# Performance work log

Hardware: AMD Instinct MI355X
Metric: run time of the kernel (lower is better)

The kernel has to match this reference:

```python
import jax, jax.numpy as jnp
import numpy as np

B, S, D, F, E, NS, K = 2, 2048, 512, 2048, 8, 2, 2


def setup_inputs() -> dict:
    key = jax.random.key(0)
    ks = jax.random.split(key, 6)
    scale = 0.02

    def p(k, shape):
        return jax.random.normal(k, shape, jnp.float32) * scale

    return {
        "x": jax.random.normal(ks[0], (B, S, D), jnp.float32),
        "gate_w": p(ks[1], (E, D)),
        "gate_b": jnp.zeros((E,), jnp.float32),
        "sw1": p(ks[2], (NS, F, D)),
        "sb1": jnp.zeros((NS, F), jnp.float32),
        "sw2": p(ks[3], (NS, D, F)),
        "sb2": jnp.zeros((NS, D), jnp.float32),
        "rw1": p(ks[4], (E, F, D)),
        "rb1": jnp.zeros((E, F), jnp.float32),
        "rw2": p(ks[5], (E, D, F)),
        "rb2": jnp.zeros((E, D), jnp.float32),
    }


def reference(x, gate_w, gate_b, sw1, sb1, sw2, sb2, rw1, rb1, rw2, rb2):
    b, s, d = x.shape
    t = x.reshape(-1, d)  # [T, D] flatten batch*seq tokens
    T = t.shape[0]

    # ---- shared experts: sum over NS FFNs (GELU exact, matching nn.GELU) ----
    hs = jax.nn.gelu(jnp.einsum('td,nfd->ntf', t, sw1) + sb1[:, None, :],
                     approximate=False)
    shared = jnp.einsum('ntf,ndf->td', hs, sw2) + sb2.sum(axis=0)

    # ---- router: softmax over experts, top-k probs/indices ----
    logits = t @ gate_w.T + gate_b               # [T, E]
    probs = jax.nn.softmax(logits, axis=-1)
    top_v, top_i = jax.lax.top_k(probs, K)       # [T, K]

    # combine weights: cw[t, e] = sum_k top_v[t, k] * (top_i[t, k] == e)
    cw = jnp.zeros_like(probs).at[jnp.arange(T)[:, None], top_i].add(top_v)  # [T, E]

    # ---- routed experts: run each expert FFN over all tokens, combine by cw ----
    # Mathematically identical to the masked gather/scatter loop in the source:
    # tokens with cw[t,e]==0 contribute nothing.
    hr = jax.nn.gelu(jnp.einsum('td,efd->etf', t, rw1) + rb1[:, None, :],
                     approximate=False)          # [E, T, F]
    oe = jnp.einsum('etf,edf->etd', hr, rw2) + rb2[:, None, :]  # [E, T, D]
    routed = jnp.einsum('etd,te->td', oe, cw)    # weighted combine

    return (shared + routed).reshape(b, s, d)
```

## Files before the change

### kernel.cpp

```cpp
#include <hip/hip_runtime.h>
#include <math.h>

typedef unsigned short u16;
typedef __attribute__((ext_vector_type(8))) __bf16 bf16x8;
typedef __attribute__((ext_vector_type(4))) float floatx4;

#define T_TOK 4096
#define DD    512
#define FF    2048
#define EE    8
#define NSH   2

#define BM 128
#define BN 128
#define BK 32
#define LDK 40
#define LDK2 32
#define BT2 64
#define CAP 4096
#define PADF 0x80000000u
#define NSLOT (2 * T_TOK + EE * BM)

__device__ __forceinline__ float bf2f(u16 v) {
  union { unsigned int u; float f; } c; c.u = ((unsigned int)v) << 16; return c.f;
}
__device__ __forceinline__ u16 f2bf(float f) {
  union { float ff; unsigned int u; } c; c.ff = f;
  unsigned int u = c.u;
  u += 0x7fffu + ((u >> 16) & 1u);
  return (u16)(u >> 16);
}
__device__ __forceinline__ float decode(const void* p, size_t idx, int f) {
  return f ? ((const float*)p)[idx] : bf2f(((const u16*)p)[idx]);
}
__device__ __forceinline__ bf16x8 load8(const void* base, size_t idx, int f) {
  if (f) {
    const float* p = (const float*)base + idx;
    float4 a = *(const float4*)p;
    float4 b = *(const float4*)(p + 4);
    union { bf16x8 v; u16 s[8]; } u;
    u.s[0] = f2bf(a.x); u.s[1] = f2bf(a.y); u.s[2] = f2bf(a.z); u.s[3] = f2bf(a.w);
    u.s[4] = f2bf(b.x); u.s[5] = f2bf(b.y); u.s[6] = f2bf(b.z); u.s[7] = f2bf(b.w);
    return u.v;
  }
  return *(const bf16x8*)((const u16*)base + idx);
}
__device__ __forceinline__ void loadf8(const void* p, size_t idx, int f,
                                       float* o) {
  if (f) {
    const float* q = (const float*)p + idx;
    float4 a = *(const float4*)q;
    float4 b = *(const float4*)(q + 4);
    o[0] = a.x; o[1] = a.y; o[2] = a.z; o[3] = a.w;
    o[4] = b.x; o[5] = b.y; o[6] = b.z; o[7] = b.w;
  } else {
    union { bf16x8 v; u16 s[8]; } u;
    u.v = *(const bf16x8*)((const u16*)p + idx);
#pragma unroll
    for (int j = 0; j < 8; ++j) o[j] = bf2f(u.s[j]);
  }
}

__device__ __forceinline__ float fast_gelu(float v) {
  float x  = v * 0.70710678118654752f;
  float ax = fabsf(x);
  float t  = __builtin_amdgcn_rcpf(fmaf(0.3275911f, ax, 1.0f));
  float p  = fmaf(t, 1.061405429f, -1.453152027f);
  p = fmaf(t, p, 1.421413741f);
  p = fmaf(t, p, -0.284496736f);
  p = fmaf(t, p, 0.254829592f);
  p = p * t;
  float e  = __expf(-ax * ax);
  float er = fmaf(-p, e, 1.0f);
  er = (x < 0.f) ? -er : er;
  return 0.5f * v * (1.0f + er);
}

__device__ __forceinline__ void gll16(const void* g, void* l) {
  __builtin_amdgcn_global_load_lds(
      (const __attribute__((address_space(1))) void*)g,
      (__attribute__((address_space(3))) void*)l, 16, 0, 0);
}
__device__ __forceinline__ void stage4(const u16* gA0, const u16* gA1,
                                       const u16* gB0, const u16* gB1,
                                       u16* Asb, u16* Bsb, int wave, int k0) {
  gll16(gA0 + k0, Asb + wave * 512);
  gll16(gA1 + k0, Asb + 2048 + wave * 512);
  gll16(gB0 + k0, Bsb + wave * 512);
  gll16(gB1 + k0, Bsb + 2048 + wave * 512);
}

__global__ __launch_bounds__(256) void detect_kernel(
    const void* x, const void* gw, const void* sw1, const void* sw2,
    const void* rw1, const void* rw2, int* flags, int* meta) {
  __shared__ int cnt;
  __shared__ int sflags[6];
  const void* ptrs[6] = {x, gw, sw1, sw2, rw1, rw2};
  for (int tnum = 0; tnum < 6; ++tnum) {
    if (threadIdx.x == 0) cnt = 0;
    __syncthreads();
    const u16* p = (const u16*)ptrs[tnum];
    int local = 0;
    for (int i = threadIdx.x; i < 4096; i += 256) {
      unsigned ef = (p[i] >> 7) & 0xFFu;
      if (ef >= 0xE0u) ++local;
    }
    if (local) atomicAdd(&cnt, local);
    __syncthreads();
    if (threadIdx.x == 0) sflags[tnum] = (cnt >= 16) ? 1 : 0;
    __syncthreads();
  }
  if (threadIdx.x == 0) {
#pragma unroll
    for (int i = 0; i < 6; ++i) flags[i] = sflags[i];
    flags[6] = sflags[0];
    flags[7] = 0;
  }
  if (meta && threadIdx.x < 24) meta[threadIdx.x] = 0;
}

__global__ __launch_bounds__(256) void conv_kernel(
    const void* __restrict__ src, u16* __restrict__ dst,
    const int* __restrict__ flags, int idx, size_t n) {
  int f = flags[idx];
  size_t i = ((size_t)blockIdx.x * 256 + threadIdx.x) * 8;
  if (i >= n) return;
  *(bf16x8*)(dst + i) = load8(src, i, f);
}

__global__ __launch_bounds__(256) void router_v(
    const void* __restrict__ x, const void* __restrict__ gw,
    const u16* __restrict__ gb, const int* __restrict__ flags,
    float* __restrict__ cw, int2* __restrict__ tix) {
  int wave = threadIdx.x >> 6, lane = threadIdx.x & 63;
  int t = blockIdx.x * 4 + wave;
  int fx = flags[0], fg = flags[1];
  float xf[8];
  loadf8(x, (size_t)t * DD + lane * 8, fx, xf);
  float acc[EE];
#pragma unroll
  for (int e = 0; e < EE; ++e) {
    float gf[8];
    loadf8(gw, (size_t)e * DD + lane * 8, fg, gf);
    float a = 0.f;
#pragma unroll
    for (int j = 0; j < 8; ++j) a = fmaf(xf[j], gf[j], a);
    acc[e] = a;
  }
#pragma unroll
  for (int e = 0; e < EE; ++e) {
    float v = acc[e];
#pragma unroll
    for (int off = 32; off > 0; off >>= 1) v += __shfl_xor(v, off, 64);
    acc[e] = v;
  }
  if (lane == 0) {
    float m = -1e30f;
#pragma unroll
    for (int e = 0; e < EE; ++e) {
      acc[e] += bf2f(gb[e]);
      m = fmaxf(m, acc[e]);
    }
    float p[EE], s = 0.f;
#pragma unroll
    for (int e = 0; e < EE; ++e) { p[e] = expf(acc[e] - m); s += p[e]; }
    int i1 = 0;
#pragma unroll
    for (int e = 1; e < EE; ++e) if (p[e] > p[i1]) i1 = e;
    int i2 = (i1 == 0) ? 1 : 0;
#pragma unroll
    for (int e = 0; e < EE; ++e)
      if (e != i1 && p[e] > p[i2]) i2 = e;
    float inv = 1.0f / s;
#pragma unroll
    for (int e = 0; e < EE; ++e)
      cw[t * EE + e] = (e == i1 || e == i2) ? p[e] * inv : 0.0f;
    tix[t] = make_int2(i1, i2);
  }
}

__global__ __launch_bounds__(256) void build_lists(
    const int2* __restrict__ tix, int* __restrict__ meta,
    unsigned* __restrict__ list, int4* __restrict__ srec) {
  int t = blockIdx.x * 256 + threadIdx.x;
  if (t >= T_TOK) return;
  int2 ii = tix[t];
  int p0 = atomicAdd(&meta[ii.x], 1);
  list[(size_t)ii.x * CAP + p0] = (unsigned)t;
  int p1 = atomicAdd(&meta[ii.y], 1);
  list[(size_t)ii.y * CAP + p1] = (unsigned)t;
  srec[t] = make_int4(ii.x, p0, ii.y, p1);
}
__global__ __launch_bounds__(256) void pad_lists(int* meta, unsigned* list) {
  if (threadIdx.x == 0) {
    int off = 0;
    for (int e = 0; e < EE; ++e) {
      int c = meta[e];
      int pc = (c + BM - 1) & ~(BM - 1);
      meta[8 + e] = pc;
      meta[16 + e] = off;
      off += pc;
    }
  }
  __syncthreads();
#pragma unroll
  for (int e = 0; e < EE; ++e) {
    int c = meta[e], pc = meta[8 + e];
    int i = c + threadIdx.x;
    if (i < pc) list[(size_t)e * CAP + i] = PADF;
  }
}


__global__ __launch_bounds__(256) void g1_fused(
    const u16* __restrict__ xb, const u16* __restrict__ s1b,
    const u16* __restrict__ sb1, const u16* __restrict__ r1b,
    const u16* __restrict__ rb1, const unsigned* __restrict__ list,
    const int* __restrict__ meta, u16* __restrict__ Hsh,
    u16* __restrict__ Hrt) {
  int z = blockIdx.z;
  int bm = blockIdx.y * BM;
  int tid = threadIdx.x, lane = tid & 63, wave = tid >> 6;
  int wm = (wave >> 1) * 64, wn = (wave & 1) * 64;
  int r = lane & 15, q = lane >> 4;
  int srow = tid >> 2, sc8 = (tid & 3) * 8;
  const int K = DD;

  __shared__ u16 As[2][BM * LDK2];
  __shared__ u16 Bs[2][BN * LDK2];

  const u16 *gA0, *gA1, *gB0;
  int e = 0, ho = 0, bn;
  if (z < 2) {
    bn = (z * 16 + blockIdx.x) * BN;
    gA0 = xb + (size_t)(bm + srow) * K + sc8;
    gA1 = gA0 + (size_t)64 * K;
    gB0 = s1b + (size_t)(bn + srow) * K + sc8;
  } else {
    e = z - 2;
    if (bm >= meta[8 + e]) return;
    ho = meta[16 + e];
    bn = blockIdx.x * BN;
    unsigned t0 = list[(size_t)e * CAP + bm + srow] & 0x7fffffffu;
    unsigned t1 = list[(size_t)e * CAP + bm + srow + 64] & 0x7fffffffu;
    gA0 = xb + (size_t)t0 * K + sc8;
    gA1 = xb + (size_t)t1 * K + sc8;
    gB0 = r1b + (size_t)e * FF * DD + (size_t)(bn + srow) * K + sc8;
  }
  const u16* gB1 = gB0 + (size_t)64 * K;

  floatx4 acc[4][4];
  floatx4 zero = {0.f, 0.f, 0.f, 0.f};
#pragma unroll
  for (int i = 0; i < 4; ++i)
#pragma unroll
    for (int j = 0; j < 4; ++j) acc[i][j] = zero;

  stage4(gA0, gA1, gB0, gB1, As[0], Bs[0], wave, 0);
  __syncthreads();
  int cur = 0;
  for (int k0 = 0; k0 < K; k0 += BK) {
    if (k0 + BK < K)
      stage4(gA0, gA1, gB0, gB1, As[cur ^ 1], Bs[cur ^ 1], wave, k0 + BK);
    bf16x8 af[4], bfr[4];
#pragma unroll
    for (int mi = 0; mi < 4; ++mi)
      af[mi] = *(const bf16x8*)(As[cur] + (wm + mi * 16 + r) * LDK2 + q * 8);
#pragma unroll
    for (int ni = 0; ni < 4; ++ni)
      bfr[ni] = *(const bf16x8*)(Bs[cur] + (wn + ni * 16 + r) * LDK2 + q * 8);
#pragma unroll
    for (int mi = 0; mi < 4; ++mi)
#pragma unroll
      for (int ni = 0; ni < 4; ++ni)
        acc[mi][ni] = __builtin_amdgcn_mfma_f32_16x16x32_bf16(
            af[mi], bfr[ni], acc[mi][ni], 0, 0, 0);
    __syncthreads();
    cur ^= 1;
  }

  if (z < 2) {
#pragma unroll
    for (int mi = 0; mi < 4; ++mi)
#pragma unroll
      for (int ni = 0; ni < 4; ++ni) {
        int col = bn + wn + ni * 16 + r;
        float bv = bf2f(sb1[col]);
#pragma unroll
        for (int rr = 0; rr < 4; ++rr) {
          int row = bm + wm + mi * 16 + q * 4 + rr;
          float v = acc[mi][ni][rr] + bv;
          Hsh[(size_t)row * (NSH * FF) + col] = f2bf(fast_gelu(v));
        }
      }
  } else {
#pragma unroll
    for (int mi = 0; mi < 4; ++mi)
#pragma unroll
      for (int ni = 0; ni < 4; ++ni) {
        int col = bn + wn + ni * 16 + r;
        float bv = bf2f(rb1[(size_t)e * FF + col]);
#pragma unroll
        for (int rr = 0; rr < 4; ++rr) {
          int slot = bm + wm + mi * 16 + q * 4 + rr;
          float v = acc[mi][ni][rr] + bv;
          Hrt[(size_t)(ho + slot) * FF + col] = f2bf(fast_gelu(v));
        }
      }
  }
}

__global__ __launch_bounds__(256) void g2_fused(
    const u16* __restrict__ Hsh, const u16* __restrict__ s2b,
    const u16* __restrict__ sb2, const u16* __restrict__ Hrt,
    const u16* __restrict__ r2b, const u16* __restrict__ rb2,
    const unsigned* __restrict__ list, const int* __restrict__ meta,
    const float* __restrict__ cw, float* __restrict__ oacc,
    float* __restrict__ Ort) {
  int z = blockIdx.z;
  int bm = blockIdx.y * BM;
  int bn = blockIdx.x * BN;
  int tid = threadIdx.x, lane = tid & 63, wave = tid >> 6;
  int wm = (wave >> 1) * 64, wn = (wave & 1) * 64;
  int r = lane & 15, q = lane >> 4;
  int srow = tid >> 2, sc8 = (tid & 3) * 8;
  const int K = FF;

  __shared__ u16 As[2][BM * LDK2];
  __shared__ u16 Bs[2][BN * LDK2];

  const u16 *gA0, *gA1, *gB0;
  int e = 0, ho = 0;
  if (z < NSH) {
    gA0 = Hsh + (size_t)(bm + srow) * (NSH * FF) + (size_t)z * FF + sc8;
    gA1 = gA0 + (size_t)64 * (NSH * FF);
    gB0 = s2b + (size_t)z * DD * FF + (size_t)(bn + srow) * K + sc8;
  } else {
    e = z - NSH;
    if (bm >= meta[8 + e]) return;
    ho = meta[16 + e];
    gA0 = Hrt + (size_t)(ho + bm + srow) * K + sc8;
    gA1 = gA0 + (size_t)64 * K;
    gB0 = r2b + (size_t)e * DD * FF + (size_t)(bn + srow) * K + sc8;
  }
  const u16* gB1 = gB0 + (size_t)64 * K;

  floatx4 acc[4][4];
  floatx4 zero = {0.f, 0.f, 0.f, 0.f};
#pragma unroll
  for (int i = 0; i < 4; ++i)
#pragma unroll
    for (int j = 0; j < 4; ++j) acc[i][j] = zero;

  stage4(gA0, gA1, gB0, gB1, As[0], Bs[0], wave, 0);
  __syncthreads();
  int cur = 0;
  for (int k0 = 0; k0 < K; k0 += BK) {
    if (k0 + BK < K)
      stage4(gA0, gA1, gB0, gB1, As[cur ^ 1], Bs[cur ^ 1], wave, k0 + BK);
    bf16x8 af[4], bfr[4];
#pragma unroll
    for (int mi = 0; mi < 4; ++mi)
      af[mi] = *(const bf16x8*)(As[cur] + (wm + mi * 16 + r) * LDK2 + q * 8);
#pragma unroll
    for (int ni = 0; ni < 4; ++ni)
      bfr[ni] = *(const bf16x8*)(Bs[cur] + (wn + ni * 16 + r) * LDK2 + q * 8);
#pragma unroll
    for (int mi = 0; mi < 4; ++mi)
#pragma unroll
      for (int ni = 0; ni < 4; ++ni)
        acc[mi][ni] = __builtin_amdgcn_mfma_f32_16x16x32_bf16(
            af[mi], bfr[ni], acc[mi][ni], 0, 0, 0);
    __syncthreads();
    cur ^= 1;
  }

  if (z < NSH) {
    float* op = oacc + (size_t)z * T_TOK * DD;
#pragma unroll
    for (int mi = 0; mi < 4; ++mi)
#pragma unroll
      for (int ni = 0; ni < 4; ++ni) {
        int col = bn + wn + ni * 16 + r;
        float bv = bf2f(sb2[(size_t)z * DD + col]);
#pragma unroll
        for (int rr = 0; rr < 4; ++rr) {
          int row = bm + wm + mi * 16 + q * 4 + rr;
          op[(size_t)row * DD + col] = acc[mi][ni][rr] + bv;
        }
      }
  } else {
#pragma unroll
    for (int mi = 0; mi < 4; ++mi)
#pragma unroll
      for (int rr = 0; rr < 4; ++rr) {
        int slot = bm + wm + mi * 16 + q * 4 + rr;
        unsigned raw = list[(size_t)e * CAP + slot];
        if (raw & PADF) continue;
        float s = cw[raw * EE + e];
#pragma unroll
        for (int ni = 0; ni < 4; ++ni) {
          int col = bn + wn + ni * 16 + r;
          float v = acc[mi][ni][rr] + bf2f(rb2[(size_t)e * DD + col]);
          Ort[(size_t)(ho + slot) * DD + col] = s * v;
        }
      }
  }
}

typedef struct { u16 a, b, c, d; } u16x4;
__global__ __launch_bounds__(256) void combine_out(
    const float* __restrict__ oacc, const float* __restrict__ Ort,
    const int4* __restrict__ srec, const int* __restrict__ meta,
    void* __restrict__ out, const int* __restrict__ flags) {
  int t  = blockIdx.x * 2 + (threadIdx.x >> 7);
  int c4 = (threadIdx.x & 127) * 4;
  int4 sr = srec[t];
  int g0 = meta[16 + sr.x] + sr.y;
  int g1 = meta[16 + sr.z] + sr.w;
  float4 a = *(const float4*)(oacc + (size_t)t * DD + c4);
  float4 b = *(const float4*)(oacc + (size_t)(T_TOK + t) * DD + c4);
  float4 u = *(const float4*)(Ort + (size_t)g0 * DD + c4);
  float4 v = *(const float4*)(Ort + (size_t)g1 * DD + c4);
  float o0 = a.x + b.x + u.x + v.x;
  float o1 = a.y + b.y + u.y + v.y;
  float o2 = a.z + b.z + u.z + v.z;
  float o3 = a.w + b.w + u.w + v.w;
  size_t idx = (size_t)t * DD + c4;
  if (flags[6]) {
    *(float4*)((float*)out + idx) = make_float4(o0, o1, o2, o3);
  } else {
    u16x4 h = {f2bf(o0), f2bf(o1), f2bf(o2), f2bf(o3)};
    *(u16x4*)((u16*)out + idx) = h;
  }
}

__device__ __forceinline__ void gemm_core(const void* A, size_t aoff, int fA,
                                          const void* B, size_t boff, int fB,
                                          int K, u16* As, u16* Bs,
                                          floatx4 acc[4][4]) {
  int tid  = threadIdx.x;
  int lane = tid & 63, wave = tid >> 6;
  int wm = (wave >> 1) * 64, wn = (wave & 1) * 64;
  int r = lane & 15, q = lane >> 4;
  int srow = tid >> 2;
  int sc8  = (tid & 3) * 8;
  size_t abase = aoff + (size_t)srow * K + sc8;
  size_t bbase = boff + (size_t)srow * K + sc8;
  const size_t half = (size_t)64 * K;

  for (int k0 = 0; k0 < K; k0 += BK) {
    bf16x8 av0 = load8(A, abase + k0, fA);
    bf16x8 av1 = load8(A, abase + half + k0, fA);
    bf16x8 bv0 = load8(B, bbase + k0, fB);
    bf16x8 bv1 = load8(B, bbase + half + k0, fB);
    __syncthreads();
    *(bf16x8*)(As + srow * LDK + sc8)        = av0;
    *(bf16x8*)(As + (srow + 64) * LDK + sc8) = av1;
    *(bf16x8*)(Bs + srow * LDK + sc8)        = bv0;
    *(bf16x8*)(Bs + (srow + 64) * LDK + sc8) = bv1;
    __syncthreads();

    bf16x8 af[4], bfr[4];
#pragma unroll
    for (int mi = 0; mi < 4; ++mi)
      af[mi] = *(const bf16x8*)(As + (wm + mi * 16 + r) * LDK + q * 8);
#pragma unroll
    for (int ni = 0; ni < 4; ++ni)
      bfr[ni] = *(const bf16x8*)(Bs + (wn + ni * 16 + r) * LDK + q * 8);
#pragma unroll
    for (int mi = 0; mi < 4; ++mi)
#pragma unroll
      for (int ni = 0; ni < 4; ++ni)
        acc[mi][ni] = __builtin_amdgcn_mfma_f32_16x16x32_bf16(
            af[mi], bfr[ni], acc[mi][ni], 0, 0, 0);
  }
}

__global__ __launch_bounds__(256) void gemm1_gelu(
    const void* __restrict__ A, size_t aoff, const void* __restrict__ B,
    size_t boff, const u16* __restrict__ bias, size_t bioff,
    u16* __restrict__ H, const int* __restrict__ flags, int iA, int iB,
    int N, int K) {
  __shared__ u16 As[BM * LDK];
  __shared__ u16 Bs[BN * LDK];
  int fA = flags[iA], fB = flags[iB];
  floatx4 acc[4][4];
  floatx4 zero = {0.f, 0.f, 0.f, 0.f};
#pragma unroll
  for (int i = 0; i < 4; ++i)
#pragma unroll
    for (int j = 0; j < 4; ++j) acc[i][j] = zero;

  int bm = blockIdx.y * BM, bn = blockIdx.x * BN;
  gemm_core(A, aoff + (size_t)bm * K, fA, B, boff + (size_t)bn * K, fB, K,
            As, Bs, acc);

  int tid = threadIdx.x, wave = tid >> 6, lane = tid & 63;
  int wm = (wave >> 1) * 64, wn = (wave & 1) * 64;
  int r = lane & 15, q = lane >> 4;
#pragma unroll
  for (int mi = 0; mi < 4; ++mi)
#pragma unroll
    for (int ni = 0; ni < 4; ++ni) {
      int col = bn + wn + ni * 16 + r;
      float bv = bf2f(bias[bioff + col]);
#pragma unroll
      for (int rr = 0; rr < 4; ++rr) {
        int row = bm + wm + mi * 16 + q * 4 + rr;
        float v = acc[mi][ni][rr] + bv;
        H[(size_t)row * N + col] = f2bf(fast_gelu(v));
      }
    }
}

__global__ __launch_bounds__(256) void gemm2_acc(
    const u16* __restrict__ A, const void* __restrict__ B, size_t boff,
    const u16* __restrict__ bias, size_t bioff, float* __restrict__ outf,
    void* __restrict__ outb, const float* __restrict__ cw,
    const int* __restrict__ flags, int iB, int expert, int accum,
    int row0, int N, int K) {
  __shared__ u16 As[BT2 * LDK];
  __shared__ u16 Bs[BT2 * LDK];
  int fB = flags[iB], fO = flags[6];
  floatx4 acc[2][2];
  floatx4 zero = {0.f, 0.f, 0.f, 0.f};
#pragma unroll
  for (int i = 0; i < 2; ++i)
#pragma unroll
    for (int j = 0; j < 2; ++j) acc[i][j] = zero;

  int bm = blockIdx.y * BT2, bn = blockIdx.x * BT2;
  int tid  = threadIdx.x;
  int lane = tid & 63, wave = tid >> 6;
  int wm = (wave >> 1) * 32, wn = (wave & 1) * 32;
  int r = lane & 15, q = lane >> 4;
  int srow = tid >> 2;
  int sc8  = (tid & 3) * 8;
  size_t abase = (size_t)(bm + srow) * K + sc8;
  size_t bbase = boff + (size_t)(bn + srow) * K + sc8;

  for (int k0 = 0; k0 < K; k0 += BK) {
    bf16x8 av = *(const bf16x8*)(A + abase + k0);
    bf16x8 bv = load8(B, bbase + k0, fB);
    __syncthreads();
    *(bf16x8*)(As + srow * LDK + sc8) = av;
    *(bf16x8*)(Bs + srow * LDK + sc8) = bv;
    __syncthreads();

    bf16x8 af[2], bfr[2];
#pragma unroll
    for (int mi = 0; mi < 2; ++mi)
      af[mi] = *(const bf16x8*)(As + (wm + mi * 16 + r) * LDK + q * 8);
#pragma unroll
    for (int ni = 0; ni < 2; ++ni)
      bfr[ni] = *(const bf16x8*)(Bs + (wn + ni * 16 + r) * LDK + q * 8);
#pragma unroll
    for (int mi = 0; mi < 2; ++mi)
#pragma unroll
      for (int ni = 0; ni < 2; ++ni)
        acc[mi][ni] = __builtin_amdgcn_mfma_f32_16x16x32_bf16(
            af[mi], bfr[ni], acc[mi][ni], 0, 0, 0);
  }

#pragma unroll
  for (int mi = 0; mi < 2; ++mi)
#pragma unroll
    for (int rr = 0; rr < 4; ++rr) {
      int grow = row0 + bm + wm + mi * 16 + q * 4 + rr;
      float s = cw ? cw[grow * EE + expert] : 1.0f;
#pragma unroll
      for (int ni = 0; ni < 2; ++ni) {
        int col = bn + wn + ni * 16 + r;
        float v = acc[mi][ni][rr] + bf2f(bias[bioff + col]);
        size_t idx = (size_t)grow * N + col;
        if (outf) {
          float prev = accum ? outf[idx] : 0.0f;
          outf[idx] = prev + s * v;
        } else if (fO) {
          float* ob = (float*)outb;
          float prev = accum ? ob[idx] : 0.0f;
          ob[idx] = prev + s * v;
        } else {
          u16* ob = (u16*)outb;
          float prev = accum ? bf2f(ob[idx]) : 0.0f;
          ob[idx] = f2bf(prev + s * v);
        }
      }
    }
}

__global__ __launch_bounds__(256) void convert_out(
    const float* __restrict__ acc, void* __restrict__ out,
    const int* __restrict__ flags, int n) {
  int i = blockIdx.x * blockDim.x + threadIdx.x;
  if (i >= n) return;
  if (flags[6]) ((float*)out)[i] = acc[i];
  else ((u16*)out)[i] = f2bf(acc[i]);
}

extern "C" void kernel_launch(void* const* d_in, const int* in_sizes, int n_in,
                              void* d_out, int out_size, void* d_ws, size_t ws_size,
                              hipStream_t stream) {
  (void)in_sizes; (void)n_in; (void)out_size;
  const void* x   = d_in[0];
  const void* gw  = d_in[1];
  const u16*  gb  = (const u16*)d_in[2];
  const void* sw1 = d_in[3];
  const u16*  sb1 = (const u16*)d_in[4];
  const void* sw2 = d_in[5];
  const u16*  sb2 = (const u16*)d_in[6];
  const void* rw1 = d_in[7];
  const u16*  rb1 = (const u16*)d_in[8];
  const void* rw2 = d_in[9];
  const u16*  rb2 = (const u16*)d_in[10];

  const size_t NX   = (size_t)T_TOK * DD;
  const size_t NW1S = (size_t)NSH * FF * DD;
  const size_t NW1R = (size_t)EE * FF * DD;
  const size_t NW2S = (size_t)NSH * DD * FF;
  const size_t NW2R = (size_t)EE * DD * FF;

  size_t off = 0;
  const size_t flO   = off; off += 256;
  const size_t cwO   = off; off += (size_t)T_TOK * EE * 4;
  const size_t tixO  = off; off += (size_t)T_TOK * 8;
  const size_t metaO = off; off += 256;
  const size_t listO = off; off += (size_t)EE * CAP * 4;
  const size_t srecO = off; off += (size_t)T_TOK * 16;
  const size_t accO  = off; off += (size_t)NSH * T_TOK * DD * 4;
  const size_t hshO  = off; off += (size_t)T_TOK * NSH * FF * 2;
  const size_t hrtO  = off; off += (size_t)NSLOT * FF * 2;
  const size_t ortO  = off; off += (size_t)NSLOT * DD * 4;
  const size_t xbO   = off; off += NX * 2;
  const size_t s1O   = off; off += NW1S * 2;
  const size_t r1O   = off; off += NW1R * 2;
  const size_t s2O   = off; off += NW2S * 2;
  const size_t r2O   = off; off += NW2R * 2;
  const int fast = (off <= ws_size) ? 1 : 0;

  char* ws = (char*)d_ws;
  int*   flags = (int*)(ws + flO);
  float* cw    = (float*)(ws + cwO);
  dim3 blk(256);

  if (fast) {
    int2*     tix  = (int2*)(ws + tixO);
    int*      meta = (int*)(ws + metaO);
    unsigned* list = (unsigned*)(ws + listO);
    int4*     srec = (int4*)(ws + srecO);
    float*    oacc = (float*)(ws + accO);
    u16*      Hsh  = (u16*)(ws + hshO);
    u16*      Hrt  = (u16*)(ws + hrtO);
    float*    Ort  = (float*)(ws + ortO);
    u16*      xb   = (u16*)(ws + xbO);
    u16*      s1b  = (u16*)(ws + s1O);
    u16*      r1b  = (u16*)(ws + r1O);
    u16*      s2b  = (u16*)(ws + s2O);
    u16*      r2b  = (u16*)(ws + r2O);

    detect_kernel<<<1, 256, 0, stream>>>(x, gw, sw1, sw2, rw1, rw2, flags,
                                         meta);
    conv_kernel<<<NX   / 2048, 256, 0, stream>>>(x,   xb,  flags, 0, NX);
    conv_kernel<<<NW1S / 2048, 256, 0, stream>>>(sw1, s1b, flags, 2, NW1S);
    conv_kernel<<<NW1R / 2048, 256, 0, stream>>>(rw1, r1b, flags, 4, NW1R);
    conv_kernel<<<NW2S / 2048, 256, 0, stream>>>(sw2, s2b, flags, 3, NW2S);
    conv_kernel<<<NW2R / 2048, 256, 0, stream>>>(rw2, r2b, flags, 5, NW2R);
    router_v<<<T_TOK / 4, 256, 0, stream>>>(x, gw, gb, flags, cw, tix);
    build_lists<<<T_TOK / 256, 256, 0, stream>>>(tix, meta, list, srec);
    pad_lists<<<1, 256, 0, stream>>>(meta, list);

    dim3 gf1(16, T_TOK / BM, 2 + EE);
    g1_fused<<<gf1, blk, 0, stream>>>(xb, s1b, sb1, r1b, rb1, list, meta,
                                      Hsh, Hrt);
    dim3 gf2(DD / BN, CAP / BM, NSH + EE);
    g2_fused<<<gf2, blk, 0, stream>>>(Hsh, s2b, sb2, Hrt, r2b, rb2, list,
                                      meta, cw, oacc, Ort);
    combine_out<<<T_TOK / 2, 256, 0, stream>>>(oacc, Ort, srec, meta, d_out,
                                               flags);
    return;
  }

  detect_kernel<<<1, 256, 0, stream>>>(x, gw, sw1, sw2, rw1, rw2, flags,
                                       nullptr);
  const size_t flB = 256, cwB = (size_t)T_TOK * EE * 4, tixB = (size_t)T_TOK * 8;
  const size_t accB = (size_t)T_TOK * DD * 4;
  static const int tcs[4] = {4096, 2048, 1024, 512};
  int TC = 0, use_f32 = 1;
  for (int i = 0; i < 4; ++i)
    if (flB + cwB + tixB + accB + (size_t)tcs[i] * FF * 2 <= ws_size) { TC = tcs[i]; break; }
  if (!TC) {
    use_f32 = 0;
    for (int i = 0; i < 4; ++i)
      if (flB + cwB + tixB + (size_t)tcs[i] * FF * 2 <= ws_size) { TC = tcs[i]; break; }
  }
  if (!TC) { TC = 512; use_f32 = 0; }

  int2*  tix     = (int2*)(ws + flB + cwB);
  float* out_acc = use_f32 ? (float*)(ws + flB + cwB + tixB) : nullptr;
  u16*   H       = (u16*)(ws + flB + cwB + tixB + (use_f32 ? accB : 0));

  router_v<<<T_TOK / 4, 256, 0, stream>>>(x, gw, gb, flags, cw, tix);
  dim3 g1(FF / BN, TC / BM);
  dim3 g2(DD / BT2, TC / BT2);
  const int nchunk = T_TOK / TC;
  for (int f = 0; f < NSH + EE; ++f) {
    const void *w1, *w2; const u16 *b1, *b2; const float* cwp;
    int expert, i1, i2v; size_t w1off, w2off, b1off, b2off;
    if (f < NSH) {
      w1 = sw1; w2 = sw2; b1 = sb1; b2 = sb2;
      w1off = (size_t)f * FF * DD; w2off = (size_t)f * DD * FF;
      b1off = (size_t)f * FF; b2off = (size_t)f * DD;
      cwp = nullptr; expert = 0; i1 = 2; i2v = 3;
    } else {
      int e = f - NSH;
      w1 = rw1; w2 = rw2; b1 = rb1; b2 = rb2;
      w1off = (size_t)e * FF * DD; w2off = (size_t)e * DD * FF;
      b1off = (size_t)e * FF; b2off = (size_t)e * DD;
      cwp = cw; expert = e; i1 = 4; i2v = 5;
    }
    int accum = (f > 0) ? 1 : 0;
    for (int c = 0; c < nchunk; ++c) {
      size_t t0 = (size_t)c * TC;
      gemm1_gelu<<<g1, blk, 0, stream>>>(x, t0 * DD, w1, w1off, b1, b1off, H,
                                         flags, 0, i1, FF, DD);
      gemm2_acc<<<g2, blk, 0, stream>>>(H, w2, w2off, b2, b2off, out_acc,
                                        d_out, cwp, flags, i2v, expert, accum,
                                        (int)t0, DD, FF);
    }
  }
  if (use_f32)
    convert_out<<<(T_TOK * DD) / 256, 256, 0, stream>>>(out_acc, d_out, flags,
                                                        T_TOK * DD);
}
```

Before: 381.5 us.

## Skip bf16 conversion when inputs are already bf16 and single-buffer GEMM LDS

The conversion kernels now return early when the detect flag says no conversion is needed. The two GEMM kernels then read the raw input pointers directly instead of the converted workspace copies, which removes a full copy pass over the weights in that case. The GEMM main loop moves into a shared helper that uses one LDS buffer with a barrier before and after each stage, instead of the double-buffered prefetch. That halves shared memory per block, which may raise occupancy, but global loads can no longer overlap the MFMA work. With fp32 inputs the conversions likely still run, so only the loss of overlap would apply.

```diff
diff --git a/kernel.cpp b/kernel.cpp
--- a/kernel.cpp
+++ b/kernel.cpp
@@ -90,6 +90,31 @@
   gll16(gB1 + k0, Bsb + 2048 + wave * 512);
 }
 
+__device__ __forceinline__ void core128(const u16* gA0, const u16* gA1,
+                                        const u16* gB0, const u16* gB1,
+                                        int K, u16* As, u16* Bs,
+                                        floatx4 acc[4][4], int wave,
+                                        int wm, int wn, int r, int q) {
+  for (int k0 = 0; k0 < K; k0 += BK) {
+    __syncthreads();
+    stage4(gA0, gA1, gB0, gB1, As, Bs, wave, k0);
+    __syncthreads();
+    bf16x8 af[4], bfr[4];
+#pragma unroll
+    for (int mi = 0; mi < 4; ++mi)
+      af[mi] = *(const bf16x8*)(As + (wm + mi * 16 + r) * LDK2 + q * 8);
+#pragma unroll
+    for (int ni = 0; ni < 4; ++ni)
+      bfr[ni] = *(const bf16x8*)(Bs + (wn + ni * 16 + r) * LDK2 + q * 8);
+#pragma unroll
+    for (int mi = 0; mi < 4; ++mi)
+#pragma unroll
+      for (int ni = 0; ni < 4; ++ni)
+        acc[mi][ni] = __builtin_amdgcn_mfma_f32_16x16x32_bf16(
+            af[mi], bfr[ni], acc[mi][ni], 0, 0, 0);
+  }
+}
+
 __global__ __launch_bounds__(256) void detect_kernel(
     const void* x, const void* gw, const void* sw1, const void* sw2,
     const void* rw1, const void* rw2, int* flags, int* meta) {
@@ -123,6 +148,7 @@
     const void* __restrict__ src, u16* __restrict__ dst,
     const int* __restrict__ flags, int idx, size_t n) {
   int f = flags[idx];
+  if (!f) return;
   size_t i = ((size_t)blockIdx.x * 256 + threadIdx.x) * 8;
   if (i >= n) return;
   *(bf16x8*)(dst + i) = load8(src, i, f);
@@ -213,11 +239,17 @@
 
 
 __global__ __launch_bounds__(256) void g1_fused(
-    const u16* __restrict__ xb, const u16* __restrict__ s1b,
-    const u16* __restrict__ sb1, const u16* __restrict__ r1b,
+    const void* __restrict__ xr, const u16* __restrict__ xb,
+    const void* __restrict__ s1r, const u16* __restrict__ s1b,
+    const u16* __restrict__ sb1,
+    const void* __restrict__ r1r, const u16* __restrict__ r1b,
     const u16* __restrict__ rb1, const unsigned* __restrict__ list,
-    const int* __restrict__ meta, u16* __restrict__ Hsh,
-    u16* __restrict__ Hrt) {
+    const int* __restrict__ meta, const int* __restrict__ flags,
+    u16* __restrict__ Hsh, u16* __restrict__ Hrt) {
+  const u16* xp  = flags[0] ? xb  : (const u16*)xr;
+  const u16* s1p = flags[2] ? s1b : (const u16*)s1r;
+  const u16* r1p = flags[4] ? r1b : (const u16*)r1r;
+
   int z = blockIdx.z;
   int bm = blockIdx.y * BM;
   int tid = threadIdx.x, lane = tid & 63, wave = tid >> 6;
@@ -226,16 +258,16 @@
   int srow = tid >> 2, sc8 = (tid & 3) * 8;
   const int K = DD;
 
-  __shared__ u16 As[2][BM * LDK2];
-  __shared__ u16 Bs[2][BN * LDK2];
+  __shared__ u16 As[BM * LDK2];
+  __shared__ u16 Bs[BN * LDK2];
 
   const u16 *gA0, *gA1, *gB0;
   int e = 0, ho = 0, bn;
   if (z < 2) {
     bn = (z * 16 + blockIdx.x) * BN;
-    gA0 = xb + (size_t)(bm + srow) * K + sc8;
+    gA0 = xp + (size_t)(bm + srow) * K + sc8;
     gA1 = gA0 + (size_t)64 * K;
-    gB0 = s1b + (size_t)(bn + srow) * K + sc8;
+    gB0 = s1p + (size_t)(bn + srow) * K + sc8;
   } else {
     e = z - 2;
     if (bm >= meta[8 + e]) return;
@@ -243,9 +275,9 @@
     bn = blockIdx.x * BN;
     unsigned t0 = list[(size_t)e * CAP + bm + srow] & 0x7fffffffu;
     unsigned t1 = list[(size_t)e * CAP + bm + srow + 64] & 0x7fffffffu;
-    gA0 = xb + (size_t)t0 * K + sc8;
-    gA1 = xb + (size_t)t1 * K + sc8;
-    gB0 = r1b + (size_t)e * FF * DD + (size_t)(bn + srow) * K + sc8;
+    gA0 = xp + (size_t)t0 * K + sc8;
+    gA1 = xp + (size_t)t1 * K + sc8;
+    gB0 = r1p + (size_t)e * FF * DD + (size_t)(bn + srow) * K + sc8;
   }
   const u16* gB1 = gB0 + (size_t)64 * K;
 
@@ -256,28 +288,7 @@
 #pragma unroll
     for (int j = 0; j < 4; ++j) acc[i][j] = zero;
 
-  stage4(gA0, gA1, gB0, gB1, As[0], Bs[0], wave, 0);
-  __syncthreads();
-  int cur = 0;
-  for (int k0 = 0; k0 < K; k0 += BK) {
-    if (k0 + BK < K)
-      stage4(gA0, gA1, gB0, gB1, As[cur ^ 1], Bs[cur ^ 1], wave, k0 + BK);
-    bf16x8 af[4], bfr[4];
-#pragma unroll
-    for (int mi = 0; mi < 4; ++mi)
-      af[mi] = *(const bf16x8*)(As[cur] + (wm + mi * 16 + r) * LDK2 + q * 8);
-#pragma unroll
-    for (int ni = 0; ni < 4; ++ni)
-      bfr[ni] = *(const bf16x8*)(Bs[cur] + (wn + ni * 16 + r) * LDK2 + q * 8);
-#pragma unroll
-    for (int mi = 0; mi < 4; ++mi)
-#pragma unroll
-      for (int ni = 0; ni < 4; ++ni)
-        acc[mi][ni] = __builtin_amdgcn_mfma_f32_16x16x32_bf16(
-            af[mi], bfr[ni], acc[mi][ni], 0, 0, 0);
-    __syncthreads();
-    cur ^= 1;
-  }
+  core128(gA0, gA1, gB0, gB1, K, As, Bs, acc, wave, wm, wn, r, q);
 
   if (z < 2) {
 #pragma unroll
@@ -311,12 +322,17 @@
 }
 
 __global__ __launch_bounds__(256) void g2_fused(
-    const u16* __restrict__ Hsh, const u16* __restrict__ s2b,
+    const u16* __restrict__ Hsh,
+    const void* __restrict__ s2r, const u16* __restrict__ s2b,
     const u16* __restrict__ sb2, const u16* __restrict__ Hrt,
-    const u16* __restrict__ r2b, const u16* __restrict__ rb2,
+    const void* __restrict__ r2r, const u16* __restrict__ r2b,
+    const u16* __restrict__ rb2,
     const unsigned* __restrict__ list, const int* __restrict__ meta,
-    const float* __restrict__ cw, float* __restrict__ oacc,
-    float* __restrict__ Ort) {
+    const int* __restrict__ flags, const float* __restrict__ cw,
+    float* __restrict__ oacc, float* __restrict__ Ort) {
+  const u16* s2p = flags[3] ? s2b : (const u16*)s2r;
+  const u16* r2p = flags[5] ? r2b : (const u16*)r2r;
+
   int z = blockIdx.z;
   int bm = blockIdx.y * BM;
   int bn = blockIdx.x * BN;
@@ -326,22 +342,22 @@
   int srow = tid >> 2, sc8 = (tid & 3) * 8;
   const int K = FF;
 
-  __shared__ u16 As[2][BM * LDK2];
-  __shared__ u16 Bs[2][BN * LDK2];
+  __shared__ u16 As[BM * LDK2];
+  __shared__ u16 Bs[BN * LDK2];
 
   const u16 *gA0, *gA1, *gB0;
   int e = 0, ho = 0;
   if (z < NSH) {
     gA0 = Hsh + (size_t)(bm + srow) * (NSH * FF) + (size_t)z * FF + sc8;
     gA1 = gA0 + (size_t)64 * (NSH * FF);
-    gB0 = s2b + (size_t)z * DD * FF + (size_t)(bn + srow) * K + sc8;
+    gB0 = s2p + (size_t)z * DD * FF + (size_t)(bn + srow) * K + sc8;
   } else {
     e = z - NSH;
     if (bm >= meta[8 + e]) return;
     ho = meta[16 + e];
     gA0 = Hrt + (size_t)(ho + bm + srow) * K + sc8;
     gA1 = gA0 + (size_t)64 * K;
-    gB0 = r2b + (size_t)e * DD * FF + (size_t)(bn + srow) * K + sc8;
+    gB0 = r2p + (size_t)e * DD * FF + (size_t)(bn + srow) * K + sc8;
   }
   const u16* gB1 = gB0 + (size_t)64 * K;
 
@@ -352,28 +368,7 @@
 #pragma unroll
     for (int j = 0; j < 4; ++j) acc[i][j] = zero;
 
-  stage4(gA0, gA1, gB0, gB1, As[0], Bs[0], wave, 0);
-  __syncthreads();
-  int cur = 0;
-  for (int k0 = 0; k0 < K; k0 += BK) {
-    if (k0 + BK < K)
-      stage4(gA0, gA1, gB0, gB1, As[cur ^ 1], Bs[cur ^ 1], wave, k0 + BK);
-    bf16x8 af[4], bfr[4];
-#pragma unroll
-    for (int mi = 0; mi < 4; ++mi)
-      af[mi] = *(const bf16x8*)(As[cur] + (wm + mi * 16 + r) * LDK2 + q * 8);
-#pragma unroll
-    for (int ni = 0; ni < 4; ++ni)
-      bfr[ni] = *(const bf16x8*)(Bs[cur] + (wn + ni * 16 + r) * LDK2 + q * 8);
-#pragma unroll
-    for (int mi = 0; mi < 4; ++mi)
-#pragma unroll
-      for (int ni = 0; ni < 4; ++ni)
-        acc[mi][ni] = __builtin_amdgcn_mfma_f32_16x16x32_bf16(
-            af[mi], bfr[ni], acc[mi][ni], 0, 0, 0);
-    __syncthreads();
-    cur ^= 1;
-  }
+  core128(gA0, gA1, gB0, gB1, K, As, Bs, acc, wave, wm, wn, r, q);
 
   if (z < NSH) {
     float* op = oacc + (size_t)z * T_TOK * DD;
@@ -671,11 +666,11 @@
     pad_lists<<<1, 256, 0, stream>>>(meta, list);
 
     dim3 gf1(16, T_TOK / BM, 2 + EE);
-    g1_fused<<<gf1, blk, 0, stream>>>(xb, s1b, sb1, r1b, rb1, list, meta,
-                                      Hsh, Hrt);
+    g1_fused<<<gf1, blk, 0, stream>>>(x, xb, sw1, s1b, sb1, rw1, r1b, rb1,
+                                      list, meta, flags, Hsh, Hrt);
     dim3 gf2(DD / BN, CAP / BM, NSH + EE);
-    g2_fused<<<gf2, blk, 0, stream>>>(Hsh, s2b, sb2, Hrt, r2b, rb2, list,
-                                      meta, cw, oacc, Ort);
+    g2_fused<<<gf2, blk, 0, stream>>>(Hsh, sw2, s2b, sb2, Hrt, rw2, r2b, rb2,
+                                      list, meta, flags, cw, oacc, Ort);
     combine_out<<<T_TOK / 2, 256, 0, stream>>>(oacc, Ort, srec, meta, d_out,
                                                flags);
     return;
```

Result: faster. 369.8 us (-3.1%).
